# Performance work log

Hardware: AMD Instinct MI355X
Metric: run time of the kernel (lower is better)

## Reference

```python
import jax, jax.numpy as jnp
import numpy as np

N, E, IN, HID, HEADS, OUT = 20000, 320000, 64, 32, 8, 128
EPS_SM = 1e-16


def setup_inputs() -> dict:
    key = jax.random.key(0)
    ks = iter(jax.random.split(key, 40))
    def g(shape, scale=0.1):
        return jax.random.normal(next(ks), shape, dtype=jnp.float32) * scale
    inp = {
        "x": jax.random.normal(next(ks), (N, IN), dtype=jnp.float32),
        "edge_index": jax.random.randint(next(ks), (2, E), 0, N, dtype=jnp.int64),
        # layer 0: GATConv(64 -> 32, heads=8, concat) => dim 256
        "W0": g((IN, HEADS * HID)), "b0": jnp.zeros((HEADS * HID,), jnp.float32),
        "as0": g((HEADS, HID)), "ad0": g((HEADS, HID)),
        "lng0": jnp.ones((HEADS * HID,), jnp.float32), "lnb0": jnp.zeros((HEADS * HID,), jnp.float32),
        "rW0": g((IN, HEADS * HID)), "rb0": jnp.zeros((HEADS * HID,), jnp.float32),
        "rw0": jnp.ones((1,), jnp.float32),
        # layer 1: GATConv(256 -> 32, heads=8, concat) => dim 256, residual = Identity
        "W1": g((HEADS * HID, HEADS * HID)), "b1": jnp.zeros((HEADS * HID,), jnp.float32),
        "as1": g((HEADS, HID)), "ad1": g((HEADS, HID)),
        "lng1": jnp.ones((HEADS * HID,), jnp.float32), "lnb1": jnp.zeros((HEADS * HID,), jnp.float32),
        "rw1": jnp.ones((1,), jnp.float32),
        # layer 2: GATConv(256 -> 128, heads=8, concat=False mean) => dim 128
        "W2": g((HEADS * HID, HEADS * OUT)), "b2": jnp.zeros((OUT,), jnp.float32),
        "as2": g((HEADS, OUT)), "ad2": g((HEADS, OUT)),
        "lng2": jnp.ones((OUT,), jnp.float32), "lnb2": jnp.zeros((OUT,), jnp.float32),
        "rW2": g((HEADS * HID, OUT)), "rb2": jnp.zeros((OUT,), jnp.float32),
        "rw2": jnp.ones((1,), jnp.float32),
    }
    return inp


def _gat_conv(x, src, dst, W, b, a_s, a_d, heads, out_c, concat):
    n = x.shape[0]
    h = (x @ W).reshape(n, heads, out_c)            # [N,H,C]
    al_s = jnp.sum(h * a_s, axis=-1)                 # [N,H]
    al_d = jnp.sum(h * a_d, axis=-1)
    e = jax.nn.leaky_relu(al_s[src] + al_d[dst], 0.2)  # [E,H]
    m = jax.ops.segment_max(e, dst, num_segments=n)
    m = jnp.where(jnp.isfinite(m), m, 0.0)
    ex = jnp.exp(e - m[dst])
    denom = jax.ops.segment_sum(ex, dst, num_segments=n)
    alpha = ex / (denom[dst] + EPS_SM)               # [E,H]
    msg = alpha[:, :, None] * h[src]                 # [E,H,C]
    out = jax.ops.segment_sum(msg, dst, num_segments=n)  # [N,H,C]
    if concat:
        return out.reshape(n, heads * out_c) + b
    return out.mean(axis=1) + b


def _layer_norm(x, g, b, eps=1e-5):
    mu = x.mean(-1, keepdims=True)
    var = x.var(-1, keepdims=True)
    return (x - mu) * jax.lax.rsqrt(var + eps) * g + b


def reference(x, edge_index, W0, b0, as0, ad0, lng0, lnb0, rW0, rb0, rw0,
              W1, b1, as1, ad1, lng1, lnb1, rw1,
              W2, b2, as2, ad2, lng2, lnb2, rW2, rb2, rw2):
    ei = edge_index.astype(jnp.int32)
    ar = jnp.arange(N, dtype=jnp.int32)
    src = jnp.concatenate([ei[0], ar])               # add self loops
    dst = jnp.concatenate([ei[1], ar])

    # layer 0 (eval mode: dropout is identity)
    g0 = _gat_conv(x, src, dst, W0, b0, as0, ad0, HEADS, HID, True)
    h = _layer_norm(g0, lng0, lnb0) + jax.nn.sigmoid(rw0) * (x @ rW0 + rb0)
    h = jax.nn.elu(h)

    # layer 1 (residual projection = Identity)
    g1 = _gat_conv(h, src, dst, W1, b1, as1, ad1, HEADS, HID, True)
    h = jax.nn.elu(_layer_norm(g1, lng1, lnb1) + jax.nn.sigmoid(rw1) * h)

    # layer 2 (concat=False -> mean over heads)
    g2 = _gat_conv(h, src, dst, W2, b2, as2, ad2, HEADS, OUT, False)
    out = _layer_norm(g2, lng2, lnb2) + jax.nn.sigmoid(rw2) * (h @ rW2 + rb2)
    return out
```

## Files before the change

kernel.cpp:

```cpp
#include <hip/hip_runtime.h>
#include <cstddef>
#include <cstdint>

#define NN 20000
#define EE 320000
#define ET (EE + NN)

typedef __attribute__((ext_vector_type(8))) short bf16x8;
typedef __attribute__((ext_vector_type(4))) float f32x4;

__device__ __forceinline__ unsigned short f2bf_rne(float f) {
  unsigned int u = __float_as_uint(f);
  u += 0x7FFF + ((u >> 16) & 1);
  return (unsigned short)(u >> 16);
}

__device__ __forceinline__ float bf2f(unsigned short b) {
  return __uint_as_float(((unsigned int)b) << 16);
}

__device__ __forceinline__ f32x4 up2(uint2 p) {
  f32x4 v = {__uint_as_float(p.x << 16), __uint_as_float(p.x & 0xFFFF0000u),
             __uint_as_float(p.y << 16), __uint_as_float(p.y & 0xFFFF0000u)};
  return v;
}


__global__ __launch_bounds__(256) void zero_i32(int* __restrict__ p, int n) {
  int i = blockIdx.x * 256 + threadIdx.x;
  if (i < n) p[i] = 0;
}

__global__ __launch_bounds__(256) void zero_f32(float* __restrict__ p, int n) {
  int i = blockIdx.x * 256 + threadIdx.x;
  if (i < n) p[i] = 0.f;
}

__global__ __launch_bounds__(256) void cvt_bf16(const float* __restrict__ src,
                                                unsigned short* __restrict__ dst, int n) {
  int i = blockIdx.x * 256 + threadIdx.x;
  if (i < n) dst[i] = f2bf_rne(src[i]);
}

__global__ void tconv(const float* __restrict__ src, unsigned short* __restrict__ dst,
                      int N) {
  int n = blockIdx.x, k = threadIdx.x, K = blockDim.x;
  dst[(size_t)n * K + k] = f2bf_rne(src[(size_t)k * N + n]);
}

__global__ void build_v16(const float* __restrict__ W2, const float* __restrict__ as2,
                          const float* __restrict__ ad2, unsigned short* __restrict__ V16) {
  int r = blockIdx.x, k = threadIdx.x;
  int h = r & 7;
  const float* av = (r < 8) ? (as2 + h * 128) : (ad2 + h * 128);
  const float* wr = W2 + (size_t)k * 1024 + h * 128;
  float v = 0.f;
#pragma unroll 4
  for (int c = 0; c < 128; ++c) v += wr[c] * av[c];
  V16[(size_t)r * 256 + k] = f2bf_rne(v);
}

__global__ void build_wstk(const float* __restrict__ W2, unsigned short* __restrict__ WT) {
  int c = blockIdx.x, k = threadIdx.x;
#pragma unroll
  for (int h = 0; h < 8; ++h)
    WT[(size_t)c * 2048 + h * 256 + k] = f2bf_rne(0.125f * W2[(size_t)k * 1024 + h * 128 + c]);
}


__global__ __launch_bounds__(256) void count_kernel(const int* __restrict__ ei,
                                                    int* __restrict__ deg) {
  int e = blockIdx.x * 256 + threadIdx.x;
  if (e < EE) {
    int d = ei[EE + e];
    if (d >= 0 && d < NN) atomicAdd(&deg[d], 1);
  }
}

__global__ __launch_bounds__(1024) void scan_blk(const int* __restrict__ deg,
    int* __restrict__ offs, int* __restrict__ bsum) {
  __shared__ int s[1024];
  int b = blockIdx.x, tid = threadIdx.x;
  int i = b * 1024 + tid;
  s[tid] = (i < NN) ? (deg[i] + 1) : 0;
  __syncthreads();
  for (int off = 1; off < 1024; off <<= 1) {
    int t = (tid >= off) ? s[tid - off] : 0;
    __syncthreads();
    s[tid] += t;
    __syncthreads();
  }
  if (i < NN) offs[i + 1] = s[tid];
  if (tid == 1023) bsum[b] = s[1023];
}

__global__ __launch_bounds__(256) void scan_add(int* __restrict__ offs,
    const int* __restrict__ bsum) {
  int i = blockIdx.x * 256 + threadIdx.x;
  if (i == 0) offs[0] = 0;
  if (i < NN) {
    int b = i >> 10;
    int pre = 0;
    for (int k = 0; k < b; ++k) pre += bsum[k];
    offs[i + 1] += pre;
  }
}

__global__ __launch_bounds__(256) void scatter_kernel(const int* __restrict__ ei,
    const int* __restrict__ offs, int* __restrict__ cursor, int* __restrict__ csr) {
  int e = blockIdx.x * 256 + threadIdx.x;
  if (e >= ET) return;
  int s, d;
  if (e < EE) { s = ei[e]; d = ei[EE + e]; }
  else        { s = e - EE; d = s; }
  if (s < 0 || s >= NN || d < 0 || d >= NN) return;
  int pos = atomicAdd(&cursor[d], 1);
  csr[offs[d] + pos] = s;
}


__global__ __launch_bounds__(256) void gemm_mfma(const unsigned short* __restrict__ A,
    const unsigned short* __restrict__ BT, const float* __restrict__ bias,
    float* __restrict__ C, int M, int K, int ldc) {
  int bm = blockIdx.y * 64, bn = blockIdx.x * 64;
  int tid = threadIdx.x;
  int w = tid >> 6, l = tid & 63;
  int wm = bm + w * 16;
  if (wm >= M) return;
  int lane16 = l & 15, q = l >> 4;
  const unsigned short* ap = A + (size_t)(wm + lane16) * K + q * 8;
  const unsigned short* bp = BT + (size_t)(bn + lane16) * K + q * 8;
  f32x4 acc0 = {0.f, 0.f, 0.f, 0.f}, acc1 = acc0, acc2 = acc0, acc3 = acc0;
#pragma unroll 2
  for (int k0 = 0; k0 < K; k0 += 32) {
    bf16x8 a  = *(const bf16x8*)(ap + k0);
    bf16x8 b0 = *(const bf16x8*)(bp + k0);
    bf16x8 b1 = *(const bf16x8*)(bp + (size_t)16 * K + k0);
    bf16x8 b2 = *(const bf16x8*)(bp + (size_t)32 * K + k0);
    bf16x8 b3 = *(const bf16x8*)(bp + (size_t)48 * K + k0);
    acc0 = __builtin_amdgcn_mfma_f32_16x16x32_bf16(a, b0, acc0, 0, 0, 0);
    acc1 = __builtin_amdgcn_mfma_f32_16x16x32_bf16(a, b1, acc1, 0, 0, 0);
    acc2 = __builtin_amdgcn_mfma_f32_16x16x32_bf16(a, b2, acc2, 0, 0, 0);
    acc3 = __builtin_amdgcn_mfma_f32_16x16x32_bf16(a, b3, acc3, 0, 0, 0);
  }
  int row0 = wm + q * 4;
  int c0 = bn + lane16;
  float bi0 = bias ? bias[c0]      : 0.f;
  float bi1 = bias ? bias[c0 + 16] : 0.f;
  float bi2 = bias ? bias[c0 + 32] : 0.f;
  float bi3 = bias ? bias[c0 + 48] : 0.f;
#pragma unroll
  for (int r = 0; r < 4; ++r) {
    float* crow = C + (size_t)(row0 + r) * ldc;
    crow[c0]      = acc0[r] + bi0;
    crow[c0 + 16] = acc1[r] + bi1;
    crow[c0 + 32] = acc2[r] + bi2;
    crow[c0 + 48] = acc3[r] + bi3;
  }
}

__global__ __launch_bounds__(256) void gemm_mfma_bf_al(const unsigned short* __restrict__ A,
    const unsigned short* __restrict__ BT, unsigned short* __restrict__ C,
    const float* __restrict__ as_w, const float* __restrict__ ad_w,
    float* __restrict__ als, float* __restrict__ ald, int M, int K) {
  int bm = blockIdx.y * 64, bn = blockIdx.x * 64;
  int tid = threadIdx.x;
  int w = tid >> 6, l = tid & 63;
  int wm = bm + w * 16;
  if (wm >= M) return;
  int lane16 = l & 15, q = l >> 4;
  const unsigned short* ap = A + (size_t)(wm + lane16) * K + q * 8;
  const unsigned short* bp = BT + (size_t)(bn + lane16) * K + q * 8;
  f32x4 acc0 = {0.f, 0.f, 0.f, 0.f}, acc1 = acc0, acc2 = acc0, acc3 = acc0;
#pragma unroll 2
  for (int k0 = 0; k0 < K; k0 += 32) {
    bf16x8 a  = *(const bf16x8*)(ap + k0);
    bf16x8 b0 = *(const bf16x8*)(bp + k0);
    bf16x8 b1 = *(const bf16x8*)(bp + (size_t)16 * K + k0);
    bf16x8 b2 = *(const bf16x8*)(bp + (size_t)32 * K + k0);
    bf16x8 b3 = *(const bf16x8*)(bp + (size_t)48 * K + k0);
    acc0 = __builtin_amdgcn_mfma_f32_16x16x32_bf16(a, b0, acc0, 0, 0, 0);
    acc1 = __builtin_amdgcn_mfma_f32_16x16x32_bf16(a, b1, acc1, 0, 0, 0);
    acc2 = __builtin_amdgcn_mfma_f32_16x16x32_bf16(a, b2, acc2, 0, 0, 0);
    acc3 = __builtin_amdgcn_mfma_f32_16x16x32_bf16(a, b3, acc3, 0, 0, 0);
  }
  int row0 = wm + q * 4;
  int c0 = bn + lane16;
#pragma unroll
  for (int r = 0; r < 4; ++r) {
    unsigned short* crow = C + (size_t)(row0 + r) * 256;
    crow[c0]      = f2bf_rne(acc0[r]);
    crow[c0 + 16] = f2bf_rne(acc1[r]);
    crow[c0 + 32] = f2bf_rne(acc2[r]);
    crow[c0 + 48] = f2bf_rne(acc3[r]);
  }
  float asA0 = as_w[c0],      asA1 = as_w[c0 + 16];
  float adA0 = ad_w[c0],      adA1 = ad_w[c0 + 16];
  float asB0 = as_w[c0 + 32], asB1 = as_w[c0 + 48];
  float adB0 = ad_w[c0 + 32], adB1 = ad_w[c0 + 48];
  int hA = (bn >> 5), hB = hA + 1;
#pragma unroll
  for (int r = 0; r < 4; ++r) {
    float sA = acc0[r] * asA0 + acc1[r] * asA1;
    float dA = acc0[r] * adA0 + acc1[r] * adA1;
    float sB = acc2[r] * asB0 + acc3[r] * asB1;
    float dB = acc2[r] * adB0 + acc3[r] * adB1;
#pragma unroll
    for (int off = 8; off >= 1; off >>= 1) {
      sA += __shfl_xor(sA, off);
      dA += __shfl_xor(dA, off);
      sB += __shfl_xor(sB, off);
      dB += __shfl_xor(dB, off);
    }
    if (lane16 == 0) {
      int row = row0 + r;
      als[row * 8 + hA] = sA;
      ald[row * 8 + hA] = dA;
      als[row * 8 + hB] = sB;
      ald[row * 8 + hB] = dB;
    }
  }
}

__global__ __launch_bounds__(256) void gemm_al16(const unsigned short* __restrict__ A,
    const unsigned short* __restrict__ V16, float* __restrict__ als,
    float* __restrict__ ald, int M) {
  int bm = blockIdx.x * 64;
  int tid = threadIdx.x;
  int w = tid >> 6, l = tid & 63;
  int wm = bm + w * 16;
  if (wm >= M) return;
  int lane16 = l & 15, q = l >> 4;
  const unsigned short* ap = A + (size_t)(wm + lane16) * 256 + q * 8;
  const unsigned short* bp = V16 + (size_t)lane16 * 256 + q * 8;
  f32x4 acc = {0.f, 0.f, 0.f, 0.f};
#pragma unroll
  for (int k0 = 0; k0 < 256; k0 += 32) {
    bf16x8 a = *(const bf16x8*)(ap + k0);
    bf16x8 b = *(const bf16x8*)(bp + k0);
    acc = __builtin_amdgcn_mfma_f32_16x16x32_bf16(a, b, acc, 0, 0, 0);
  }
  int row0 = wm + q * 4;
  float* dst = (lane16 < 8) ? als : ald;
  int h = lane16 & 7;
#pragma unroll
  for (int r = 0; r < 4; ++r)
    dst[(size_t)(row0 + r) * 8 + h] = acc[r];
}


__global__ __launch_bounds__(256) void gemm_y_tiled(const unsigned short* __restrict__ A,
    const unsigned short* __restrict__ BT, float* __restrict__ P, int M) {
  __shared__ unsigned short sA[64][72];
  __shared__ unsigned short sB[128][72];
  int bm = blockIdx.x * 64, s = blockIdx.y;
  int tid = threadIdx.x;
  int w = tid >> 6, l = tid & 63;
  int lane16 = l & 15, q = l >> 4;
  int soff = s * 512;
  int r = tid >> 3, c = (tid & 7) * 8;
  int rA0 = min(bm + r, M - 1);
  int rA1 = min(bm + r + 32, M - 1);
  f32x4 acc[8] = {};
#pragma unroll 1
  for (int kt = 0; kt < 8; ++kt) {
    int kb = soff + kt * 64 + c;
    *(bf16x8*)&sA[r][c]      = *(const bf16x8*)(A + (size_t)rA0 * 2048 + kb);
    *(bf16x8*)&sA[r + 32][c] = *(const bf16x8*)(A + (size_t)rA1 * 2048 + kb);
#pragma unroll
    for (int rr = 0; rr < 4; ++rr)
      *(bf16x8*)&sB[r + rr * 32][c] = *(const bf16x8*)(BT + (size_t)(r + rr * 32) * 2048 + kb);
    __syncthreads();
#pragma unroll
    for (int kk = 0; kk < 2; ++kk) {
      bf16x8 a = *(const bf16x8*)&sA[w * 16 + lane16][kk * 32 + q * 8];
#pragma unroll
      for (int t = 0; t < 8; ++t) {
        bf16x8 b = *(const bf16x8*)&sB[t * 16 + lane16][kk * 32 + q * 8];
        acc[t] = __builtin_amdgcn_mfma_f32_16x16x32_bf16(a, b, acc[t], 0, 0, 0);
      }
    }
    __syncthreads();
  }
  int row0 = bm + w * 16 + q * 4;
  float* pbase = P + (size_t)s * ((size_t)M * 128);
#pragma unroll
  for (int r2 = 0; r2 < 4; ++r2) {
    if (row0 + r2 < M) {
      float* prow = pbase + (size_t)(row0 + r2) * 128 + lane16;
#pragma unroll
      for (int t = 0; t < 8; ++t) prow[t * 16] = acc[t][r2];
    }
  }
}


__global__ __launch_bounds__(256) void al2(const float* __restrict__ h,
    const float* __restrict__ aw_s, const float* __restrict__ aw_d,
    float* __restrict__ als, float* __restrict__ ald) {
  int n = blockIdx.x, tid = threadIdx.x;
  int j = tid & 127;
  __shared__ float ss[256], sd[256];
  float v = h[(size_t)n * 256 + tid];
  ss[tid] = v * aw_s[tid];
  sd[tid] = v * aw_d[tid];
  __syncthreads();
  for (int off = 64; off > 0; off >>= 1) {
    if (j < off) { ss[tid] += ss[tid + off]; sd[tid] += sd[tid + off]; }
    __syncthreads();
  }
  if (j == 0) {
    int hh = tid >> 7;
    als[n * 2 + hh] = ss[tid];
    ald[n * 2 + hh] = sd[tid];
  }
}


__global__ __launch_bounds__(256) void agg_epi_w(const unsigned short* __restrict__ hG,
    const float* __restrict__ als, const float* __restrict__ ald,
    const int* __restrict__ offs, const int* __restrict__ csr,
    const float* __restrict__ bias, const float* __restrict__ lng,
    const float* __restrict__ lnb, const float* __restrict__ resf,
    const unsigned short* __restrict__ resb, const float* __restrict__ rw,
    unsigned short* __restrict__ outbf) {
  int w = threadIdx.x >> 6, l = threadIdx.x & 63;
  int n = blockIdx.x * 4 + w;
  if (n >= NN) return;
  int r0 = offs[n], r1 = offs[n + 1], deg = r1 - r0;
  int h8 = l & 7, e8 = l >> 3, hl = l >> 3;
  float aldn = ald[n * 8 + h8];
  f32x4 acc = {0.f, 0.f, 0.f, 0.f};
  float den = 0.f;
  for (int c0 = 0; c0 < deg; c0 += 8) {
    int cn = min(8, deg - c0);
    int src_my = csr[r0 + c0 + min(e8, cn - 1)];
    float ev = als[src_my * 8 + h8] + aldn;
    ev = ev >= 0.f ? ev : 0.2f * ev;
    float aexp = (e8 < cn) ? __expf(ev) : 0.f;
#pragma unroll 2
    for (int e = 0; e < cn; ++e) {
      int s = __shfl(src_my, e * 8);
      float a = __shfl(aexp, e * 8 + hl);
      uint2 p = *(const uint2*)(hG + (size_t)s * 256 + l * 4);
      acc += a * up2(p);
      den += a;
    }
  }
  float dinv = 1.f / (den + 1e-16f);
  float4 bi = ((const float4*)bias)[l];
  f32x4 rr;
  if (resf) {
    float4 t = ((const float4*)resf)[(size_t)n * 64 + l];
    rr.x = t.x; rr.y = t.y; rr.z = t.z; rr.w = t.w;
  } else {
    uint2 pb = ((const uint2*)resb)[(size_t)n * 64 + l];
    rr = up2(pb);
  }
  f32x4 val = {acc.x * dinv + bi.x, acc.y * dinv + bi.y,
               acc.z * dinv + bi.z, acc.w * dinv + bi.w};
  float v1 = val.x + val.y + val.z + val.w;
  float v2 = val.x * val.x + val.y * val.y + val.z * val.z + val.w * val.w;
#pragma unroll
  for (int off = 32; off >= 1; off >>= 1) {
    v1 += __shfl_xor(v1, off);
    v2 += __shfl_xor(v2, off);
  }
  float mu = v1 * (1.f / 256.f);
  float var = v2 * (1.f / 256.f) - mu * mu;
  float rs = rsqrtf(var + 1e-5f);
  float sig = 1.f / (1.f + __expf(-rw[0]));
  float4 lg = ((const float4*)lng)[l];
  float4 lb = ((const float4*)lnb)[l];
  float ov[4];
  const float* valp = (const float*)&val;
  const float* rrp = (const float*)&rr;
  const float* lgp = &lg.x;
  const float* lbp = &lb.x;
#pragma unroll
  for (int k = 0; k < 4; ++k) {
    float rv = (valp[k] - mu) * rs * lgp[k] + lbp[k] + sig * rrp[k];
    ov[k] = rv > 0.f ? rv : (__expf(rv) - 1.f);
  }
  uint2 pk;
  pk.x = (unsigned)f2bf_rne(ov[0]) | ((unsigned)f2bf_rne(ov[1]) << 16);
  pk.y = (unsigned)f2bf_rne(ov[2]) | ((unsigned)f2bf_rne(ov[3]) << 16);
  ((uint2*)outbf)[(size_t)n * 64 + l] = pk;
}


__global__ __launch_bounds__(256) void agg_y_w(const unsigned short* __restrict__ hbf,
    const float* __restrict__ als, const float* __restrict__ ald,
    const int* __restrict__ offs, const int* __restrict__ csr,
    unsigned short* __restrict__ Y) {
  int w = threadIdx.x >> 6, l = threadIdx.x & 63;
  int n = blockIdx.x * 4 + w;
  if (n >= NN) return;
  int r0 = offs[n], r1 = offs[n + 1], deg = r1 - r0;
  int h8 = l & 7, e8 = l >> 3;
  float aldn = ald[n * 8 + h8];
  f32x4 accv[8] = {};
  float den[8] = {};
  for (int c0 = 0; c0 < deg; c0 += 8) {
    int cn = min(8, deg - c0);
    int src_my = csr[r0 + c0 + min(e8, cn - 1)];
    float ev = als[src_my * 8 + h8] + aldn;
    ev = ev >= 0.f ? ev : 0.2f * ev;
    float aexp = (e8 < cn) ? __expf(ev) : 0.f;
    for (int e = 0; e < cn; ++e) {
      int s = __shfl(src_my, e * 8);
      uint2 p = *(const uint2*)(hbf + (size_t)s * 256 + l * 4);
      f32x4 v = up2(p);
#pragma unroll
      for (int h = 0; h < 8; ++h) {
        float a = __shfl(aexp, e * 8 + h);
        accv[h] += a * v;
        den[h] += a;
      }
    }
  }
  unsigned short* yrow = Y + (size_t)n * 2048;
#pragma unroll
  for (int h = 0; h < 8; ++h) {
    float sc = 1.f / (den[h] + 1e-16f);
    f32x4 t = accv[h];
    uint2 pk;
    pk.x = (unsigned)f2bf_rne(t.x * sc) | ((unsigned)f2bf_rne(t.y * sc) << 16);
    pk.y = (unsigned)f2bf_rne(t.z * sc) | ((unsigned)f2bf_rne(t.w * sc) << 16);
    *(uint2*)(yrow + h * 256 + l * 4) = pk;
  }
}


__global__ __launch_bounds__(256) void agg2_pair(const float* __restrict__ h2,
    const float* __restrict__ als, const float* __restrict__ ald,
    const int* __restrict__ offs, const int* __restrict__ csr,
    float* __restrict__ acc_out) {
  int n = blockIdx.x, tid = threadIdx.x;
  int r0 = offs[n], r1 = offs[n + 1];
  __shared__ float s_red[256];
  __shared__ float s_dn[2];
  int hh = tid >> 7, j = tid & 127;
  float aldn = ald[n * 2 + hh];
  float sm = 0.f;
  for (int i = r0 + j; i < r1; i += 128) {
    int s = csr[i];
    float ev = als[s * 2 + hh] + aldn;
    ev = ev >= 0.f ? ev : 0.2f * ev;
    sm += __expf(ev);
  }
  s_red[tid] = sm;
  __syncthreads();
  for (int off = 64; off > 0; off >>= 1) {
    if (j < off) s_red[tid] += s_red[tid + off];
    __syncthreads();
  }
  if (j == 0) s_dn[hh] = s_red[tid] + 1e-16f;
  __syncthreads();
  float dinv = 1.f / s_dn[hh];
  float acc = 0.f;
  for (int i = r0; i < r1; ++i) {
    int s = csr[i];
    float ev = als[s * 2 + hh] + aldn;
    ev = ev >= 0.f ? ev : 0.2f * ev;
    float alpha = __expf(ev) * dinv;
    acc += alpha * h2[(size_t)s * 256 + tid];
  }
  s_red[tid] = acc;
  __syncthreads();
  if (tid < 128)
    acc_out[(size_t)n * 128 + tid] += 0.125f * (s_red[tid] + s_red[tid + 128]);
}


__global__ __launch_bounds__(128) void epi_out_res4(const float* __restrict__ P,
    const float* __restrict__ b2, const float* __restrict__ lng,
    const float* __restrict__ lnb, const float* __restrict__ res2,
    const float* __restrict__ rw, float* __restrict__ out) {
  int n = blockIdx.x, tid = threadIdx.x;
  __shared__ float sw1[2], sw2[2];
  size_t stride = (size_t)NN * 128;
  size_t idx = (size_t)n * 128 + tid;
  float g = P[idx] + P[stride + idx] + P[2 * stride + idx] + P[3 * stride + idx] + b2[tid];
  float v1 = g, v2 = g * g;
#pragma unroll
  for (int off = 32; off >= 1; off >>= 1) {
    v1 += __shfl_xor(v1, off);
    v2 += __shfl_xor(v2, off);
  }
  if ((tid & 63) == 0) { sw1[tid >> 6] = v1; sw2[tid >> 6] = v2; }
  __syncthreads();
  float tot1 = sw1[0] + sw1[1], tot2 = sw2[0] + sw2[1];
  float mu = tot1 * (1.f / 128.f);
  float var = tot2 * (1.f / 128.f) - mu * mu;
  float rs = rsqrtf(var + 1e-5f);
  float sig = 1.f / (1.f + __expf(-rw[0]));
  out[idx] = (g - mu) * rs * lng[tid] + lnb[tid] + sig * res2[idx];
}

__global__ __launch_bounds__(128) void epi_out_res(float* __restrict__ acc,
    const float* __restrict__ b2, const float* __restrict__ lng,
    const float* __restrict__ lnb, const float* __restrict__ res2,
    const float* __restrict__ rw) {
  int n = blockIdx.x, tid = threadIdx.x;
  __shared__ float s1[128], s2[128];
  __shared__ float s_mu, s_rs;
  float g = acc[(size_t)n * 128 + tid] + b2[tid];
  s1[tid] = g; s2[tid] = g * g;
  __syncthreads();
  for (int off = 64; off > 0; off >>= 1) {
    if (tid < off) { s1[tid] += s1[tid + off]; s2[tid] += s2[tid + off]; }
    __syncthreads();
  }
  if (tid == 0) {
    float mu = s1[0] * (1.f / 128.f);
    float var = s2[0] * (1.f / 128.f) - mu * mu;
    s_mu = mu; s_rs = rsqrtf(var + 1e-5f);
  }
  __syncthreads();
  float sig = 1.f / (1.f + __expf(-rw[0]));
  float lnv = (g - s_mu) * s_rs * lng[tid] + lnb[tid];
  acc[(size_t)n * 128 + tid] = lnv + sig * res2[(size_t)n * 128 + tid];
}

__global__ __launch_bounds__(128) void epi_out_mv(float* __restrict__ acc,
    const float* __restrict__ b2, const float* __restrict__ lng,
    const float* __restrict__ lnb, const unsigned short* __restrict__ hB,
    const float* __restrict__ rW2, const float* __restrict__ rb2,
    const float* __restrict__ rw) {
  int n = blockIdx.x, tid = threadIdx.x;
  __shared__ float srow[256];
  __shared__ float s1[128], s2[128];
  __shared__ float s_mu, s_rs;
  srow[tid] = bf2f(hB[(size_t)n * 256 + tid]);
  srow[tid + 128] = bf2f(hB[(size_t)n * 256 + tid + 128]);
  float g = acc[(size_t)n * 128 + tid] + b2[tid];
  s1[tid] = g; s2[tid] = g * g;
  __syncthreads();
  for (int off = 64; off > 0; off >>= 1) {
    if (tid < off) { s1[tid] += s1[tid + off]; s2[tid] += s2[tid + off]; }
    __syncthreads();
  }
  if (tid == 0) {
    float mu = s1[0] * (1.f / 128.f);
    float var = s2[0] * (1.f / 128.f) - mu * mu;
    s_mu = mu; s_rs = rsqrtf(var + 1e-5f);
  }
  __syncthreads();
  float rv = rb2[tid];
#pragma unroll 4
  for (int k = 0; k < 256; ++k) rv += srow[k] * rW2[(size_t)k * 128 + tid];
  float sig = 1.f / (1.f + __expf(-rw[0]));
  float lnv = (g - s_mu) * s_rs * lng[tid] + lnb[tid];
  acc[(size_t)n * 128 + tid] = lnv + sig * rv;
}


extern "C" void kernel_launch(void* const* d_in, const int* in_sizes, int n_in,
                              void* d_out, int out_size, void* d_ws, size_t ws_size,
                              hipStream_t stream) {
  const float* x   = (const float*)d_in[0];
  const int*   ei  = (const int*)d_in[1];
  const float* W0  = (const float*)d_in[2];
  const float* b0  = (const float*)d_in[3];
  const float* as0 = (const float*)d_in[4];
  const float* ad0 = (const float*)d_in[5];
  const float* lng0= (const float*)d_in[6];
  const float* lnb0= (const float*)d_in[7];
  const float* rW0 = (const float*)d_in[8];
  const float* rb0 = (const float*)d_in[9];
  const float* rw0 = (const float*)d_in[10];
  const float* W1  = (const float*)d_in[11];
  const float* b1  = (const float*)d_in[12];
  const float* as1 = (const float*)d_in[13];
  const float* ad1 = (const float*)d_in[14];
  const float* lng1= (const float*)d_in[15];
  const float* lnb1= (const float*)d_in[16];
  const float* rw1 = (const float*)d_in[17];
  const float* W2  = (const float*)d_in[18];
  const float* b2  = (const float*)d_in[19];
  const float* as2 = (const float*)d_in[20];
  const float* ad2 = (const float*)d_in[21];
  const float* lng2= (const float*)d_in[22];
  const float* lnb2= (const float*)d_in[23];
  const float* rW2 = (const float*)d_in[24];
  const float* rb2 = (const float*)d_in[25];
  const float* rw2 = (const float*)d_in[26];
  float* outp = (float*)d_out;

  char* w = (char*)d_ws;
  auto carve = [&](size_t bytes) -> char* {
    char* p = w;
    w += (bytes + 255) & ~(size_t)255;
    return p;
  };
  float* bufH = (float*)carve((size_t)NN * 256 * 4);
  float* bufR = (float*)carve((size_t)NN * 256 * 4);
  float* als  = (float*)carve((size_t)NN * 8 * 4);
  float* ald  = (float*)carve((size_t)NN * 8 * 4);
  int* deg    = (int*)carve((size_t)2 * NN * 4);
  int* cursor = deg + NN;
  int* offs   = (int*)carve((size_t)(NN + 1) * 4);
  int* bsum   = (int*)carve((size_t)32 * 4);
  int* csr    = (int*)carve((size_t)ET * 4);
  unsigned short* xbf  = (unsigned short*)carve((size_t)NN * 64 * 2);
  unsigned short* hbf0 = (unsigned short*)carve((size_t)NN * 256 * 2);
  unsigned short* hbf1 = (unsigned short*)carve((size_t)NN * 256 * 2);
  unsigned short* W0T  = (unsigned short*)carve((size_t)256 * 64 * 2);
  unsigned short* rW0T = (unsigned short*)carve((size_t)256 * 64 * 2);
  unsigned short* W1T  = (unsigned short*)carve((size_t)256 * 256 * 2);
  unsigned short* W2T  = (unsigned short*)carve((size_t)1024 * 256 * 2);
  unsigned short* rW2T = (unsigned short*)carve((size_t)128 * 256 * 2);
  size_t base = (size_t)(w - (char*)d_ws);
  if (ws_size < base) return;
  unsigned short* hG = (unsigned short*)bufH;

  size_t full_extra = (((size_t)16 * 256 * 2 + 255) & ~(size_t)255)
                    + (((size_t)128 * 2048 * 2 + 255) & ~(size_t)255)
                    + (((size_t)NN * 2048 * 2 + 255) & ~(size_t)255);
  size_t res2_extra = (((size_t)NN * 128 * 4 + 255) & ~(size_t)255);
  bool full = (ws_size - base) >= full_extra;
  unsigned short *V16 = nullptr, *WstkT = nullptr, *Ybuf = nullptr;
  if (full) {
    V16   = (unsigned short*)carve((size_t)16 * 256 * 2);
    WstkT = (unsigned short*)carve((size_t)128 * 2048 * 2);
    Ybuf  = (unsigned short*)carve((size_t)NN * 2048 * 2);
  }
  float* res2 = nullptr;
  if ((ws_size - (size_t)(w - (char*)d_ws)) >= res2_extra)
    res2 = (float*)carve((size_t)NN * 128 * 4);

  zero_i32<<<(2 * NN + 255) / 256, 256, 0, stream>>>(deg, 2 * NN);
  count_kernel<<<(EE + 255) / 256, 256, 0, stream>>>(ei, deg);
  int nb = (NN + 1023) / 1024;
  scan_blk<<<nb, 1024, 0, stream>>>(deg, offs, bsum);
  scan_add<<<(NN + 255) / 256, 256, 0, stream>>>(offs, bsum);
  scatter_kernel<<<(ET + 255) / 256, 256, 0, stream>>>(ei, offs, cursor, csr);

  cvt_bf16<<<(NN * 64 + 255) / 256, 256, 0, stream>>>(x, xbf, NN * 64);
  tconv<<<256, 64, 0, stream>>>(W0, W0T, 256);
  tconv<<<256, 64, 0, stream>>>(rW0, rW0T, 256);
  tconv<<<256, 256, 0, stream>>>(W1, W1T, 256);
  tconv<<<128, 256, 0, stream>>>(rW2, rW2T, 128);
  if (full) {
    build_v16<<<16, 256, 0, stream>>>(W2, as2, ad2, V16);
    build_wstk<<<128, 256, 0, stream>>>(W2, WstkT);
  } else {
    tconv<<<1024, 256, 0, stream>>>(W2, W2T, 1024);
  }

  dim3 g256(4, (NN + 63) / 64);
  dim3 g128(2, (NN + 63) / 64);
  int gagg = (NN + 3) / 4;

  gemm_mfma_bf_al<<<g256, 256, 0, stream>>>(xbf, W0T, hG, as0, ad0, als, ald, NN, 64);
  gemm_mfma<<<g256, 256, 0, stream>>>(xbf, rW0T, rb0, bufR, NN, 64, 256);
  agg_epi_w<<<gagg, 256, 0, stream>>>(hG, als, ald, offs, csr, b0, lng0, lnb0,
                                      bufR, nullptr, rw0, hbf0);

  gemm_mfma_bf_al<<<g256, 256, 0, stream>>>(hbf0, W1T, hG, as1, ad1, als, ald, NN, 256);
  agg_epi_w<<<gagg, 256, 0, stream>>>(hG, als, ald, offs, csr, b1, lng1, lnb1,
                                      nullptr, hbf0, rw1, hbf1);

  if (res2)
    gemm_mfma<<<g128, 256, 0, stream>>>(hbf1, rW2T, rb2, res2, NN, 256, 128);
  if (full) {
    gemm_al16<<<(NN + 63) / 64, 256, 0, stream>>>(hbf1, V16, als, ald, NN);
    agg_y_w<<<gagg, 256, 0, stream>>>(hbf1, als, ald, offs, csr, Ybuf);
    if (res2) {
      float* partial = bufH;
      gemm_y_tiled<<<dim3((NN + 63) / 64, 4), 256, 0, stream>>>(Ybuf, WstkT,
                                                                partial, NN);
      epi_out_res4<<<NN, 128, 0, stream>>>(partial, b2, lng2, lnb2, res2, rw2, outp);
    } else {
      gemm_mfma<<<g128, 256, 0, stream>>>(Ybuf, WstkT, nullptr, outp, NN, 2048, 128);
      epi_out_mv<<<NN, 128, 0, stream>>>(outp, b2, lng2, lnb2, hbf1, rW2, rb2, rw2);
    }
  } else {
    zero_f32<<<(NN * 128 + 255) / 256, 256, 0, stream>>>(outp, NN * 128);
    for (int p = 0; p < 4; ++p) {
      gemm_mfma<<<g256, 256, 0, stream>>>(hbf1, W2T + (size_t)p * 256 * 256, nullptr,
                                          bufH, NN, 256, 256);
      al2<<<NN, 256, 0, stream>>>(bufH, as2 + p * 256, ad2 + p * 256, als, ald);
      agg2_pair<<<NN, 256, 0, stream>>>(bufH, als, ald, offs, csr, outp);
    }
    if (res2)
      epi_out_res<<<NN, 128, 0, stream>>>(outp, b2, lng2, lnb2, res2, rw2);
    else
      epi_out_mv<<<NN, 128, 0, stream>>>(outp, b2, lng2, lnb2, hbf1, rW2, rb2, rw2);
  }
}
```

Measured before the change: 423.2 us.

## Split layer-2 aggregation across two waves per node and store residual in bf16

The layer-2 Y aggregation now uses two waves per node, each handling four heads with 16 edges per chunk. This halves the per-lane accumulator registers and shuffle count per edge, at the cost of reading neighbour features twice. The layer-0 residual projection now writes bf16 into a reused buffer instead of fp32, halving its store and reload traffic at some precision cost. Softmax denominators are accumulated once per chunk and reduced by butterfly shuffles instead of being summed per edge.

```diff
diff --git a/kernel.cpp b/kernel.cpp
--- a/kernel.cpp
+++ b/kernel.cpp
@@ -156,6 +156,43 @@
     crow[c0 + 16] = acc1[r] + bi1;
     crow[c0 + 32] = acc2[r] + bi2;
     crow[c0 + 48] = acc3[r] + bi3;
+  }
+}
+
+__global__ __launch_bounds__(256) void gemm_mfma_bf_bias(const unsigned short* __restrict__ A,
+    const unsigned short* __restrict__ BT, const float* __restrict__ bias,
+    unsigned short* __restrict__ C, int M, int K, int ldc) {
+  int bm = blockIdx.y * 64, bn = blockIdx.x * 64;
+  int tid = threadIdx.x;
+  int w = tid >> 6, l = tid & 63;
+  int wm = bm + w * 16;
+  if (wm >= M) return;
+  int lane16 = l & 15, q = l >> 4;
+  const unsigned short* ap = A + (size_t)(wm + lane16) * K + q * 8;
+  const unsigned short* bp = BT + (size_t)(bn + lane16) * K + q * 8;
+  f32x4 acc0 = {0.f, 0.f, 0.f, 0.f}, acc1 = acc0, acc2 = acc0, acc3 = acc0;
+#pragma unroll 2
+  for (int k0 = 0; k0 < K; k0 += 32) {
+    bf16x8 a  = *(const bf16x8*)(ap + k0);
+    bf16x8 b0 = *(const bf16x8*)(bp + k0);
+    bf16x8 b1 = *(const bf16x8*)(bp + (size_t)16 * K + k0);
+    bf16x8 b2 = *(const bf16x8*)(bp + (size_t)32 * K + k0);
+    bf16x8 b3 = *(const bf16x8*)(bp + (size_t)48 * K + k0);
+    acc0 = __builtin_amdgcn_mfma_f32_16x16x32_bf16(a, b0, acc0, 0, 0, 0);
+    acc1 = __builtin_amdgcn_mfma_f32_16x16x32_bf16(a, b1, acc1, 0, 0, 0);
+    acc2 = __builtin_amdgcn_mfma_f32_16x16x32_bf16(a, b2, acc2, 0, 0, 0);
+    acc3 = __builtin_amdgcn_mfma_f32_16x16x32_bf16(a, b3, acc3, 0, 0, 0);
+  }
+  int row0 = wm + q * 4;
+  int c0 = bn + lane16;
+  float bi0 = bias[c0], bi1 = bias[c0 + 16], bi2 = bias[c0 + 32], bi3 = bias[c0 + 48];
+#pragma unroll
+  for (int r = 0; r < 4; ++r) {
+    unsigned short* crow = C + (size_t)(row0 + r) * ldc;
+    crow[c0]      = f2bf_rne(acc0[r] + bi0);
+    crow[c0 + 16] = f2bf_rne(acc1[r] + bi1);
+    crow[c0 + 32] = f2bf_rne(acc2[r] + bi2);
+    crow[c0 + 48] = f2bf_rne(acc3[r] + bi3);
   }
 }
 
@@ -321,9 +358,8 @@
     const float* __restrict__ als, const float* __restrict__ ald,
     const int* __restrict__ offs, const int* __restrict__ csr,
     const float* __restrict__ bias, const float* __restrict__ lng,
-    const float* __restrict__ lnb, const float* __restrict__ resf,
-    const unsigned short* __restrict__ resb, const float* __restrict__ rw,
-    unsigned short* __restrict__ outbf) {
+    const float* __restrict__ lnb, const unsigned short* __restrict__ resb,
+    const float* __restrict__ rw, unsigned short* __restrict__ outbf) {
   int w = threadIdx.x >> 6, l = threadIdx.x & 63;
   int n = blockIdx.x * 4 + w;
   if (n >= NN) return;
@@ -331,32 +367,30 @@
   int h8 = l & 7, e8 = l >> 3, hl = l >> 3;
   float aldn = ald[n * 8 + h8];
   f32x4 acc = {0.f, 0.f, 0.f, 0.f};
-  float den = 0.f;
+  float denacc = 0.f;
   for (int c0 = 0; c0 < deg; c0 += 8) {
     int cn = min(8, deg - c0);
     int src_my = csr[r0 + c0 + min(e8, cn - 1)];
     float ev = als[src_my * 8 + h8] + aldn;
     ev = ev >= 0.f ? ev : 0.2f * ev;
     float aexp = (e8 < cn) ? __expf(ev) : 0.f;
+    denacc += aexp;
 #pragma unroll 2
     for (int e = 0; e < cn; ++e) {
       int s = __shfl(src_my, e * 8);
       float a = __shfl(aexp, e * 8 + hl);
       uint2 p = *(const uint2*)(hG + (size_t)s * 256 + l * 4);
       acc += a * up2(p);
-      den += a;
     }
   }
+  denacc += __shfl_xor(denacc, 8);
+  denacc += __shfl_xor(denacc, 16);
+  denacc += __shfl_xor(denacc, 32);
+  float den = __shfl(denacc, hl);
   float dinv = 1.f / (den + 1e-16f);
   float4 bi = ((const float4*)bias)[l];
-  f32x4 rr;
-  if (resf) {
-    float4 t = ((const float4*)resf)[(size_t)n * 64 + l];
-    rr.x = t.x; rr.y = t.y; rr.z = t.z; rr.w = t.w;
-  } else {
-    uint2 pb = ((const uint2*)resb)[(size_t)n * 64 + l];
-    rr = up2(pb);
-  }
+  uint2 pb = ((const uint2*)resb)[(size_t)n * 64 + l];
+  f32x4 rr = up2(pb);
   f32x4 val = {acc.x * dinv + bi.x, acc.y * dinv + bi.y,
                acc.z * dinv + bi.z, acc.w * dinv + bi.w};
   float v1 = val.x + val.y + val.z + val.w;
@@ -389,40 +423,47 @@
 }
 
 
-__global__ __launch_bounds__(256) void agg_y_w(const unsigned short* __restrict__ hbf,
+__global__ __launch_bounds__(256) void agg_y_w2(const unsigned short* __restrict__ hbf,
     const float* __restrict__ als, const float* __restrict__ ald,
     const int* __restrict__ offs, const int* __restrict__ csr,
     unsigned short* __restrict__ Y) {
   int w = threadIdx.x >> 6, l = threadIdx.x & 63;
-  int n = blockIdx.x * 4 + w;
+  int n = blockIdx.x * 2 + (w >> 1);
+  int half = w & 1;
   if (n >= NN) return;
   int r0 = offs[n], r1 = offs[n + 1], deg = r1 - r0;
-  int h8 = l & 7, e8 = l >> 3;
-  float aldn = ald[n * 8 + h8];
-  f32x4 accv[8] = {};
-  float den[8] = {};
-  for (int c0 = 0; c0 < deg; c0 += 8) {
-    int cn = min(8, deg - c0);
-    int src_my = csr[r0 + c0 + min(e8, cn - 1)];
-    float ev = als[src_my * 8 + h8] + aldn;
+  int e16 = l >> 2;
+  int hh = half * 4 + (l & 3);
+  float aldn = ald[n * 8 + hh];
+  f32x4 accv[4] = {};
+  float denacc = 0.f;
+  for (int c0 = 0; c0 < deg; c0 += 16) {
+    int cn = min(16, deg - c0);
+    int src_my = csr[r0 + c0 + min(e16, cn - 1)];
+    float ev = als[src_my * 8 + hh] + aldn;
     ev = ev >= 0.f ? ev : 0.2f * ev;
-    float aexp = (e8 < cn) ? __expf(ev) : 0.f;
+    float aexp = (e16 < cn) ? __expf(ev) : 0.f;
+    denacc += aexp;
     for (int e = 0; e < cn; ++e) {
-      int s = __shfl(src_my, e * 8);
+      int s = __shfl(src_my, e * 4);
       uint2 p = *(const uint2*)(hbf + (size_t)s * 256 + l * 4);
       f32x4 v = up2(p);
 #pragma unroll
-      for (int h = 0; h < 8; ++h) {
-        float a = __shfl(aexp, e * 8 + h);
+      for (int h = 0; h < 4; ++h) {
+        float a = __shfl(aexp, e * 4 + h);
         accv[h] += a * v;
-        den[h] += a;
       }
     }
   }
-  unsigned short* yrow = Y + (size_t)n * 2048;
-#pragma unroll
-  for (int h = 0; h < 8; ++h) {
-    float sc = 1.f / (den[h] + 1e-16f);
+  denacc += __shfl_xor(denacc, 4);
+  denacc += __shfl_xor(denacc, 8);
+  denacc += __shfl_xor(denacc, 16);
+  denacc += __shfl_xor(denacc, 32);
+  unsigned short* yrow = Y + (size_t)n * 2048 + (size_t)half * 1024;
+#pragma unroll
+  for (int h = 0; h < 4; ++h) {
+    float dh = __shfl(denacc, h);
+    float sc = 1.f / (dh + 1e-16f);
     f32x4 t = accv[h];
     uint2 pk;
     pk.x = (unsigned)f2bf_rne(t.x * sc) | ((unsigned)f2bf_rne(t.y * sc) << 16);
@@ -652,21 +693,22 @@
   dim3 g256(4, (NN + 63) / 64);
   dim3 g128(2, (NN + 63) / 64);
   int gagg = (NN + 3) / 4;
+  int gagg2 = (NN + 1) / 2;
 
   gemm_mfma_bf_al<<<g256, 256, 0, stream>>>(xbf, W0T, hG, as0, ad0, als, ald, NN, 64);
-  gemm_mfma<<<g256, 256, 0, stream>>>(xbf, rW0T, rb0, bufR, NN, 64, 256);
+  gemm_mfma_bf_bias<<<g256, 256, 0, stream>>>(xbf, rW0T, rb0, hbf1, NN, 64, 256);
   agg_epi_w<<<gagg, 256, 0, stream>>>(hG, als, ald, offs, csr, b0, lng0, lnb0,
-                                      bufR, nullptr, rw0, hbf0);
+                                      hbf1, rw0, hbf0);
 
   gemm_mfma_bf_al<<<g256, 256, 0, stream>>>(hbf0, W1T, hG, as1, ad1, als, ald, NN, 256);
   agg_epi_w<<<gagg, 256, 0, stream>>>(hG, als, ald, offs, csr, b1, lng1, lnb1,
-                                      nullptr, hbf0, rw1, hbf1);
+                                      hbf0, rw1, hbf1);
 
   if (res2)
     gemm_mfma<<<g128, 256, 0, stream>>>(hbf1, rW2T, rb2, res2, NN, 256, 128);
   if (full) {
     gemm_al16<<<(NN + 63) / 64, 256, 0, stream>>>(hbf1, V16, als, ald, NN);
-    agg_y_w<<<gagg, 256, 0, stream>>>(hbf1, als, ald, offs, csr, Ybuf);
+    agg_y_w2<<<gagg2, 256, 0, stream>>>(hbf1, als, ald, offs, csr, Ybuf);
     if (res2) {
       float* partial = bufH;
       gemm_y_tiled<<<dim3((NN + 63) / 64, 4), 256, 0, stream>>>(Ybuf, WstkT,
```

Result: no change. 426.1 us (+0.7%).
